# Optimization experiments

Measured on AMD Instinct MI355X. Metric: run time of the kernel, lower is better.

Reference implementation:

```python
import jax, jax.numpy as jnp
import numpy as np

BETA = 1.0  # inverse temperature (default of retrieve())
EPS = 1e-12  # matches torch F.normalize eps


def _l2_normalize(x):
    # torch.nn.functional.normalize(p=2, dim=-1): x / max(||x||, eps)
    n = jnp.sqrt(jnp.sum(x * x, axis=-1, keepdims=True))
    return x / jnp.maximum(n, EPS)


def setup_inputs() -> dict:
    key = jax.random.key(0)
    kq, kk = jax.random.split(key)
    N, K, D = 65536, 4096, 128
    queries = jax.random.normal(kq, (N, D), dtype=jnp.float32)
    # learnable memory keys, init_std = 0.02
    keys = jax.random.normal(kk, (K, D), dtype=jnp.float32) * 0.02
    return {"queries": queries, "keys": keys}


def reference(queries, keys):
    # normalize_keys=True, normalize_queries=True
    k_n = _l2_normalize(keys)
    q_n = _l2_normalize(queries)
    # values are TIED to the raw keys parameter (get_values returns self.keys,
    # un-normalized) — only the score-side keys are normalized.
    values = keys
    scores = BETA * jnp.einsum('nd,kd->nk', q_n, k_n)  # [N, K]
    attention = jax.nn.softmax(scores, axis=-1)
    retrieved = jnp.einsum('nk,kd->nd', attention, values)  # [N, D]
    return retrieved
```

## Files before the change

kernel.cpp:

```cpp
#include <hip/hip_runtime.h>
#include <hip/hip_bf16.h>
#include <stdint.h>


typedef __attribute__((ext_vector_type(8))) short bf16x8;
typedef __attribute__((ext_vector_type(16))) float f32x16;

#define MFMA32(a, b, c) __builtin_amdgcn_mfma_f32_32x32x16_bf16(a, b, c, 0, 0, 0)
#define ASYNC_CP16(gsrc, ldst)                                                  \
  __builtin_amdgcn_global_load_lds(                                             \
      (const __attribute__((address_space(1))) void*)(gsrc),                    \
      (__attribute__((address_space(3))) void*)(ldst), 16, 0, 0)

__device__ __forceinline__ unsigned pkbf(float lo, float hi) {
  union { __hip_bfloat162 h2; unsigned u; } v;
  v.h2 = __float22bfloat162_rn(float2{lo, hi});
  return v.u;
}

__global__ __launch_bounds__(256) void prep_k(const float* __restrict__ k,
                                              char* __restrict__ knf,
                                              char* __restrict__ vtf, int K) {
  __shared__ float sRaw[64 * 132];
  __shared__ float sScale[64];
  const int tid = threadIdx.x;
  const int kbase = blockIdx.x * 64;
  {
    const int key_loc = tid >> 2, dq = tid & 3;
    const float4* src = (const float4*)(k + (size_t)(kbase + key_loc) * 128 + dq * 32);
    float4 f[8];
    float ss = 0.f;
#pragma unroll
    for (int i = 0; i < 8; ++i) {
      f[i] = src[i];
      ss += f[i].x * f[i].x + f[i].y * f[i].y + f[i].z * f[i].z + f[i].w * f[i].w;
    }
    ss += __shfl_xor(ss, 1);
    ss += __shfl_xor(ss, 2);
    float4* dst = (float4*)(sRaw + key_loc * 132 + dq * 32);
#pragma unroll
    for (int i = 0; i < 8; ++i) dst[i] = f[i];
    if (dq == 0) sScale[key_loc] = ss > 0.f ? rsqrtf(ss) : 0.f;
  }
  __syncthreads();

#pragma unroll
  for (int r = 0; r < 4; ++r) {
    const int c = r * 256 + tid;
    const int t_loc = c >> 9, ds = (c >> 6) & 7, l = c & 63;
    const int h5 = l >> 5, c32 = l & 31;
    const int key_loc = t_loc * 32 + c32;
    const float sc = sScale[key_loc];
    const float* p = sRaw + key_loc * 132 + ds * 16 + h5 * 8;
    uint4 w;
    w.x = pkbf(p[0] * sc, p[1] * sc);
    w.y = pkbf(p[2] * sc, p[3] * sc);
    w.z = pkbf(p[4] * sc, p[5] * sc);
    w.w = pkbf(p[6] * sc, p[7] * sc);
    *(uint4*)(knf + ((size_t)blockIdx.x * 1024 + c) * 16) = w;
  }
#pragma unroll
  for (int r = 0; r < 4; ++r) {
    const int c = r * 256 + tid;
    const int s = c >> 8, db2 = (c >> 6) & 3, l = c & 63;
    const int h5 = l >> 5, c32 = l & 31;
    const int d = db2 * 32 + c32;
    const int kb = (s >> 1) * 32 + (s & 1) * 8 + h5 * 4;
    float f[8];
#pragma unroll
    for (int j = 0; j < 8; ++j)
      f[j] = sRaw[(kb + (j & 3) + (j >> 2) * 16) * 132 + d];
    uint4 w;
    w.x = pkbf(f[0], f[1]);
    w.y = pkbf(f[2], f[3]);
    w.z = pkbf(f[4], f[5]);
    w.w = pkbf(f[6], f[7]);
    *(uint4*)(vtf + ((size_t)blockIdx.x * 1024 + c) * 16) = w;
  }
}

__global__ __launch_bounds__(256, 2) void attn_main(
    const float* __restrict__ q, const char* __restrict__ knf,
    const char* __restrict__ vtf, float* __restrict__ out, int K) {
  __shared__ __align__(16) char sK[2][16384];
  const int tid = threadIdx.x;
  const int wave = tid >> 6, lane = tid & 63;
  const int h5 = lane >> 5, c32 = lane & 31;
  const int qrow0 = blockIdx.x * 128 + wave * 32;

  bf16x8 qf[8];
  {
    const float* qr = q + (size_t)(qrow0 + c32) * 128;
    float f[64];
    float ss = 0.f;
#pragma unroll
    for (int ds = 0; ds < 8; ++ds) {
      const float4 a = *(const float4*)(qr + ds * 16 + h5 * 8);
      const float4 b = *(const float4*)(qr + ds * 16 + h5 * 8 + 4);
      f[ds * 8 + 0] = a.x; f[ds * 8 + 1] = a.y; f[ds * 8 + 2] = a.z; f[ds * 8 + 3] = a.w;
      f[ds * 8 + 4] = b.x; f[ds * 8 + 5] = b.y; f[ds * 8 + 6] = b.z; f[ds * 8 + 7] = b.w;
    }
#pragma unroll
    for (int i = 0; i < 64; ++i) ss += f[i] * f[i];
    ss += __shfl_xor(ss, 32);
    const float sc = (ss > 0.f ? rsqrtf(ss) : 0.f) * 1.44269504f;
#pragma unroll
    for (int ds = 0; ds < 8; ++ds) {
      union { unsigned u[4]; bf16x8 v; } t;
#pragma unroll
      for (int p = 0; p < 4; ++p)
        t.u[p] = pkbf(f[ds * 8 + 2 * p] * sc, f[ds * 8 + 2 * p + 1] * sc);
      qf[ds] = t.v;
    }
  }

  f32x16 acc[4];
#pragma unroll
  for (int db2 = 0; db2 < 4; ++db2)
#pragma unroll
    for (int r = 0; r < 16; ++r) acc[db2][r] = 0.f;
  float den = 0.f;

  const int nIter = K >> 6;
  auto stage = [&](int it, int buf) {
#pragma unroll
    for (int i = 0; i < 4; ++i)
      ASYNC_CP16(knf + (size_t)it * 16384 + (wave * 4 + i) * 1024 + lane * 16,
                 sK[buf] + (wave * 4 + i) * 1024);
  };

  stage(0, 0);
  for (int it = 0; it < nIter; ++it) {
    const int buf = it & 1;
    __syncthreads();
    if (it + 1 < nIter) stage(it + 1, buf ^ 1);

    f32x16 S[2];
#pragma unroll
    for (int t = 0; t < 2; ++t) {
      f32x16 s;
#pragma unroll
      for (int r = 0; r < 16; ++r) s[r] = 0.f;
#pragma unroll
      for (int ds = 0; ds < 8; ++ds) {
        const bf16x8 kf = *(const bf16x8*)(sK[buf] + (t * 8 + ds) * 1024 + lane * 16);
        s = MFMA32(kf, qf[ds], s);
      }
      S[t] = s;
    }

    const char* vbase = vtf + (size_t)it * 16384;
    bf16x8 vcur[4], vnxt[4];
#pragma unroll
    for (int db2 = 0; db2 < 4; ++db2)
      vcur[db2] = *(const bf16x8*)(vbase + db2 * 1024 + lane * 16);
#pragma unroll
    for (int s = 0; s < 4; ++s) {
      if (s < 3)
#pragma unroll
        for (int db2 = 0; db2 < 4; ++db2)
          vnxt[db2] = *(const bf16x8*)(vbase + ((s + 1) * 4 + db2) * 1024 + lane * 16);
      const int t = s >> 1, w = s & 1;
      float e[8];
#pragma unroll
      for (int j = 0; j < 8; ++j) {
        const int rr = w * 4 + (j & 3) + (j >> 2) * 8;
        e[j] = __builtin_amdgcn_exp2f(S[t][rr]);
      }
      den += ((e[0] + e[1]) + (e[2] + e[3])) + ((e[4] + e[5]) + (e[6] + e[7]));
      union { unsigned u[4]; bf16x8 v; } pf;
#pragma unroll
      for (int j2 = 0; j2 < 4; ++j2) pf.u[j2] = pkbf(e[2 * j2], e[2 * j2 + 1]);
#pragma unroll
      for (int db2 = 0; db2 < 4; ++db2)
        acc[db2] = MFMA32(vcur[db2], pf.v, acc[db2]);
      if (s < 3)
#pragma unroll
        for (int db2 = 0; db2 < 4; ++db2) vcur[db2] = vnxt[db2];
    }
  }

  den += __shfl_xor(den, 32);
  const float rd = 1.0f / den;

  __syncthreads();
  float* wls = (float*)(&sK[0][0] + wave * 4096);
#pragma unroll
  for (int db2 = 0; db2 < 4; ++db2) {
#pragma unroll
    for (int qd = 0; qd < 4; ++qd) {
      float4 v;
      v.x = acc[db2][qd * 4 + 0] * rd;
      v.y = acc[db2][qd * 4 + 1] * rd;
      v.z = acc[db2][qd * 4 + 2] * rd;
      v.w = acc[db2][qd * 4 + 3] * rd;
      *(float4*)(wls + c32 * 32 + (((h5 + 2 * qd) ^ (c32 & 7)) << 2)) = v;
    }
#pragma unroll
    for (int p = 0; p < 4; ++p) {
      const int ql = p * 8 + (lane >> 3);
      const int x = lane & 7;
      const float4 v = *(const float4*)(wls + ql * 32 + ((x ^ (ql & 7)) << 2));
      *(float4*)(out + (size_t)(qrow0 + ql) * 128 + db2 * 32 + x * 4) = v;
    }
  }
}

extern "C" void kernel_launch(void* const* d_in, const int* in_sizes, int n_in,
                              void* d_out, int out_size, void* d_ws, size_t ws_size,
                              hipStream_t stream) {
  const float* q = (const float*)d_in[0];
  const float* k = (const float*)d_in[1];
  const int N = in_sizes[0] / 128;
  const int K = in_sizes[1] / 128;
  char* ws = (char*)d_ws;
  char* knf = ws;
  char* vtf = ws + (size_t)K * 256;
  float* out = (float*)d_out;

  prep_k<<<dim3(K / 64), dim3(256), 0, stream>>>(k, knf, vtf, K);
  attn_main<<<dim3(N / 128), dim3(256), 0, stream>>>(q, knf, vtf, out, K);
}
```

Baseline: 222.2 us.

## Shrink attention blocks to two waves and process 32 keys per iteration

The main kernel now runs 128-thread blocks covering 64 query rows each, with twice as many blocks, and walks the key dimension 32 keys at a time with 8KB LDS stages instead of 64 keys with 16KB stages. This lowers register and LDS use per block, letting more blocks sit on a CU and shortening each loop body's score live range. The cost is twice as many barriers and iterations, each key tile being reused by only two waves, and more global traffic for the streamed V tiles and K staging.

```diff
diff --git a/kernel.cpp b/kernel.cpp
--- a/kernel.cpp
+++ b/kernel.cpp
@@ -79,14 +79,14 @@
   }
 }
 
-__global__ __launch_bounds__(256, 2) void attn_main(
+__global__ __launch_bounds__(128, 4) void attn_main(
     const float* __restrict__ q, const char* __restrict__ knf,
     const char* __restrict__ vtf, float* __restrict__ out, int K) {
-  __shared__ __align__(16) char sK[2][16384];
+  __shared__ __align__(16) char sK[2][8192];
   const int tid = threadIdx.x;
   const int wave = tid >> 6, lane = tid & 63;
   const int h5 = lane >> 5, c32 = lane & 31;
-  const int qrow0 = blockIdx.x * 128 + wave * 32;
+  const int qrow0 = blockIdx.x * 64 + wave * 32;
 
   bf16x8 qf[8];
   {
@@ -120,13 +120,18 @@
 #pragma unroll
     for (int r = 0; r < 16; ++r) acc[db2][r] = 0.f;
   float den = 0.f;
-
-  const int nIter = K >> 6;
+  f32x16 Zf;
+#pragma unroll
+  for (int r = 0; r < 16; ++r) Zf[r] = 0.f;
+
+  const int nIter = K >> 5;
   auto stage = [&](int it, int buf) {
 #pragma unroll
-    for (int i = 0; i < 4; ++i)
-      ASYNC_CP16(knf + (size_t)it * 16384 + (wave * 4 + i) * 1024 + lane * 16,
-                 sK[buf] + (wave * 4 + i) * 1024);
+    for (int i = 0; i < 4; ++i) {
+      const int ii = wave * 4 + i;
+      ASYNC_CP16(knf + (size_t)it * 8192 + ii * 1024 + lane * 16,
+                 sK[buf] + ii * 1024);
+    }
   };
 
   stage(0, 0);
@@ -135,37 +140,30 @@
     __syncthreads();
     if (it + 1 < nIter) stage(it + 1, buf ^ 1);
 
-    f32x16 S[2];
-#pragma unroll
-    for (int t = 0; t < 2; ++t) {
-      f32x16 s;
-#pragma unroll
-      for (int r = 0; r < 16; ++r) s[r] = 0.f;
-#pragma unroll
-      for (int ds = 0; ds < 8; ++ds) {
-        const bf16x8 kf = *(const bf16x8*)(sK[buf] + (t * 8 + ds) * 1024 + lane * 16);
-        s = MFMA32(kf, qf[ds], s);
-      }
-      S[t] = s;
-    }
-
-    const char* vbase = vtf + (size_t)it * 16384;
+    const char* vbase = vtf + (size_t)it * 8192;
     bf16x8 vcur[4], vnxt[4];
 #pragma unroll
     for (int db2 = 0; db2 < 4; ++db2)
       vcur[db2] = *(const bf16x8*)(vbase + db2 * 1024 + lane * 16);
-#pragma unroll
-    for (int s = 0; s < 4; ++s) {
-      if (s < 3)
+
+    f32x16 S;
+#pragma unroll
+    for (int ds = 0; ds < 8; ++ds) {
+      const bf16x8 kf = *(const bf16x8*)(sK[buf] + ds * 1024 + lane * 16);
+      S = MFMA32(kf, qf[ds], (ds == 0) ? Zf : S);
+    }
+
+#pragma unroll
+    for (int s = 0; s < 2; ++s) {
+      if (s == 0)
 #pragma unroll
         for (int db2 = 0; db2 < 4; ++db2)
-          vnxt[db2] = *(const bf16x8*)(vbase + ((s + 1) * 4 + db2) * 1024 + lane * 16);
-      const int t = s >> 1, w = s & 1;
+          vnxt[db2] = *(const bf16x8*)(vbase + (4 + db2) * 1024 + lane * 16);
       float e[8];
 #pragma unroll
       for (int j = 0; j < 8; ++j) {
-        const int rr = w * 4 + (j & 3) + (j >> 2) * 8;
-        e[j] = __builtin_amdgcn_exp2f(S[t][rr]);
+        const int rr = s * 4 + (j & 3) + (j >> 2) * 8;
+        e[j] = __builtin_amdgcn_exp2f(S[rr]);
       }
       den += ((e[0] + e[1]) + (e[2] + e[3])) + ((e[4] + e[5]) + (e[6] + e[7]));
       union { unsigned u[4]; bf16x8 v; } pf;
@@ -174,7 +172,7 @@
 #pragma unroll
       for (int db2 = 0; db2 < 4; ++db2)
         acc[db2] = MFMA32(vcur[db2], pf.v, acc[db2]);
-      if (s < 3)
+      if (s == 0)
 #pragma unroll
         for (int db2 = 0; db2 < 4; ++db2) vcur[db2] = vnxt[db2];
     }
@@ -219,5 +217,5 @@
   float* out = (float*)d_out;
 
   prep_k<<<dim3(K / 64), dim3(256), 0, stream>>>(k, knf, vtf, K);
-  attn_main<<<dim3(N / 128), dim3(256), 0, stream>>>(q, knf, vtf, out, K);
-}
+  attn_main<<<dim3(N / 64), dim3(128), 0, stream>>>(q, knf, vtf, out, K);
+}
```

Measured after the change: 399.8 us. 1.8x slower.

## Software-pipeline QK scores, exp and PV across key-block iterations

Applied to the files above, without the earlier changes.

Splits the loop body into score computation, exponentiation and PV accumulation. It then skews them so the PV MFMAs of the previous key block are issued between the current block's QK MFMAs and its exp work. The goal is to overlap transcendental and packing ALU work with matrix-core work instead of running them serially inside one iteration. It also seeds the first QK MFMA from a zero constant instead of re-zeroing the accumulator. In exchange it keeps four packed probability fragments live across iterations, which raises register pressure, and it adds a peeled prologue and epilogue.

```diff
diff --git a/kernel.cpp b/kernel.cpp
--- a/kernel.cpp
+++ b/kernel.cpp
@@ -120,6 +120,12 @@
 #pragma unroll
     for (int r = 0; r < 16; ++r) acc[db2][r] = 0.f;
   float den = 0.f;
+  f32x16 Zf;
+#pragma unroll
+  for (int r = 0; r < 16; ++r) Zf[r] = 0.f;
+
+  union pfu { unsigned u[4]; bf16x8 v; };
+  pfu pf[4];
 
   const int nIter = K >> 6;
   auto stage = [&](int it, int buf) {
@@ -129,27 +135,21 @@
                  sK[buf] + (wave * 4 + i) * 1024);
   };
 
-  stage(0, 0);
-  for (int it = 0; it < nIter; ++it) {
-    const int buf = it & 1;
-    __syncthreads();
-    if (it + 1 < nIter) stage(it + 1, buf ^ 1);
-
-    f32x16 S[2];
+  auto computeS = [&](int buf, f32x16* S) {
 #pragma unroll
     for (int t = 0; t < 2; ++t) {
       f32x16 s;
 #pragma unroll
-      for (int r = 0; r < 16; ++r) s[r] = 0.f;
-#pragma unroll
       for (int ds = 0; ds < 8; ++ds) {
         const bf16x8 kf = *(const bf16x8*)(sK[buf] + (t * 8 + ds) * 1024 + lane * 16);
-        s = MFMA32(kf, qf[ds], s);
+        s = MFMA32(kf, qf[ds], (ds == 0) ? Zf : s);
       }
       S[t] = s;
     }
-
-    const char* vbase = vtf + (size_t)it * 16384;
+  };
+
+  auto doPV = [&](int m) {
+    const char* vbase = vtf + (size_t)m * 16384;
     bf16x8 vcur[4], vnxt[4];
 #pragma unroll
     for (int db2 = 0; db2 < 4; ++db2)
@@ -160,6 +160,18 @@
 #pragma unroll
         for (int db2 = 0; db2 < 4; ++db2)
           vnxt[db2] = *(const bf16x8*)(vbase + ((s + 1) * 4 + db2) * 1024 + lane * 16);
+#pragma unroll
+      for (int db2 = 0; db2 < 4; ++db2)
+        acc[db2] = MFMA32(vcur[db2], pf[s].v, acc[db2]);
+      if (s < 3)
+#pragma unroll
+        for (int db2 = 0; db2 < 4; ++db2) vcur[db2] = vnxt[db2];
+    }
+  };
+
+  auto doExp = [&](const f32x16* S) {
+#pragma unroll
+    for (int s = 0; s < 4; ++s) {
       const int t = s >> 1, w = s & 1;
       float e[8];
 #pragma unroll
@@ -168,17 +180,29 @@
         e[j] = __builtin_amdgcn_exp2f(S[t][rr]);
       }
       den += ((e[0] + e[1]) + (e[2] + e[3])) + ((e[4] + e[5]) + (e[6] + e[7]));
-      union { unsigned u[4]; bf16x8 v; } pf;
-#pragma unroll
-      for (int j2 = 0; j2 < 4; ++j2) pf.u[j2] = pkbf(e[2 * j2], e[2 * j2 + 1]);
-#pragma unroll
-      for (int db2 = 0; db2 < 4; ++db2)
-        acc[db2] = MFMA32(vcur[db2], pf.v, acc[db2]);
-      if (s < 3)
-#pragma unroll
-        for (int db2 = 0; db2 < 4; ++db2) vcur[db2] = vnxt[db2];
-    }
-  }
+#pragma unroll
+      for (int j2 = 0; j2 < 4; ++j2) pf[s].u[j2] = pkbf(e[2 * j2], e[2 * j2 + 1]);
+    }
+  };
+
+  stage(0, 0);
+  __syncthreads();
+  stage(1, 1);
+  {
+    f32x16 S[2];
+    computeS(0, S);
+    doExp(S);
+  }
+  for (int it = 1; it < nIter; ++it) {
+    const int buf = it & 1;
+    __syncthreads();
+    if (it + 1 < nIter) stage(it + 1, buf ^ 1);
+    f32x16 S[2];
+    computeS(buf, S);
+    doPV(it - 1);
+    doExp(S);
+  }
+  doPV(nIter - 1);
 
   den += __shfl_xor(den, 32);
   const float rd = 1.0f / den;
```

Measured after the change: 221.5 us. No clear change (-0.3%).

## Split key dimension across two blocks with separate reduction kernel

Applied to the files above, without the earlier changes.

Splits the K loop into two halves handled by separate blocks (gridDim.y=2). Each half writes unnormalized numerators and denominators, and a new reduce kernel sums and normalizes them. Occupancy is raised to 3 blocks per SU, and the V register double-buffering is removed to free registers. The cost is extra global traffic for a second N×128 numerator, the denominators, and one more launch.

```diff
diff --git a/kernel.cpp b/kernel.cpp
--- a/kernel.cpp
+++ b/kernel.cpp
@@ -79,13 +79,15 @@
   }
 }
 
-__global__ __launch_bounds__(256, 2) void attn_main(
+__global__ __launch_bounds__(256, 3) void attn_main(
     const float* __restrict__ q, const char* __restrict__ knf,
-    const char* __restrict__ vtf, float* __restrict__ out, int K) {
+    const char* __restrict__ vtf, float* __restrict__ num0,
+    float* __restrict__ num1, float* __restrict__ den, int N, int K) {
   __shared__ __align__(16) char sK[2][16384];
   const int tid = threadIdx.x;
   const int wave = tid >> 6, lane = tid & 63;
   const int h5 = lane >> 5, c32 = lane & 31;
+  const int split = blockIdx.y;
   const int qrow0 = blockIdx.x * 128 + wave * 32;
 
   bf16x8 qf[8];
@@ -119,47 +121,41 @@
   for (int db2 = 0; db2 < 4; ++db2)
 #pragma unroll
     for (int r = 0; r < 16; ++r) acc[db2][r] = 0.f;
-  float den = 0.f;
-
-  const int nIter = K >> 6;
-  auto stage = [&](int it, int buf) {
+  float denv = 0.f;
+  f32x16 Zf;
+#pragma unroll
+  for (int r = 0; r < 16; ++r) Zf[r] = 0.f;
+
+  const int iBeg = split * (K >> 7);
+  const int nIter = K >> 7;
+  auto stage = [&](int m, int buf) {
 #pragma unroll
     for (int i = 0; i < 4; ++i)
-      ASYNC_CP16(knf + (size_t)it * 16384 + (wave * 4 + i) * 1024 + lane * 16,
+      ASYNC_CP16(knf + (size_t)m * 16384 + (wave * 4 + i) * 1024 + lane * 16,
                  sK[buf] + (wave * 4 + i) * 1024);
   };
 
-  stage(0, 0);
+  stage(iBeg, 0);
   for (int it = 0; it < nIter; ++it) {
     const int buf = it & 1;
     __syncthreads();
-    if (it + 1 < nIter) stage(it + 1, buf ^ 1);
+    if (it + 1 < nIter) stage(iBeg + it + 1, buf ^ 1);
 
     f32x16 S[2];
 #pragma unroll
     for (int t = 0; t < 2; ++t) {
       f32x16 s;
 #pragma unroll
-      for (int r = 0; r < 16; ++r) s[r] = 0.f;
-#pragma unroll
       for (int ds = 0; ds < 8; ++ds) {
         const bf16x8 kf = *(const bf16x8*)(sK[buf] + (t * 8 + ds) * 1024 + lane * 16);
-        s = MFMA32(kf, qf[ds], s);
+        s = MFMA32(kf, qf[ds], (ds == 0) ? Zf : s);
       }
       S[t] = s;
     }
 
-    const char* vbase = vtf + (size_t)it * 16384;
-    bf16x8 vcur[4], vnxt[4];
-#pragma unroll
-    for (int db2 = 0; db2 < 4; ++db2)
-      vcur[db2] = *(const bf16x8*)(vbase + db2 * 1024 + lane * 16);
+    const char* vbase = vtf + (size_t)(iBeg + it) * 16384;
 #pragma unroll
     for (int s = 0; s < 4; ++s) {
-      if (s < 3)
-#pragma unroll
-        for (int db2 = 0; db2 < 4; ++db2)
-          vnxt[db2] = *(const bf16x8*)(vbase + ((s + 1) * 4 + db2) * 1024 + lane * 16);
       const int t = s >> 1, w = s & 1;
       float e[8];
 #pragma unroll
@@ -167,21 +163,21 @@
         const int rr = w * 4 + (j & 3) + (j >> 2) * 8;
         e[j] = __builtin_amdgcn_exp2f(S[t][rr]);
       }
-      den += ((e[0] + e[1]) + (e[2] + e[3])) + ((e[4] + e[5]) + (e[6] + e[7]));
+      denv += ((e[0] + e[1]) + (e[2] + e[3])) + ((e[4] + e[5]) + (e[6] + e[7]));
       union { unsigned u[4]; bf16x8 v; } pf;
 #pragma unroll
       for (int j2 = 0; j2 < 4; ++j2) pf.u[j2] = pkbf(e[2 * j2], e[2 * j2 + 1]);
 #pragma unroll
-      for (int db2 = 0; db2 < 4; ++db2)
-        acc[db2] = MFMA32(vcur[db2], pf.v, acc[db2]);
-      if (s < 3)
-#pragma unroll
-        for (int db2 = 0; db2 < 4; ++db2) vcur[db2] = vnxt[db2];
-    }
-  }
-
-  den += __shfl_xor(den, 32);
-  const float rd = 1.0f / den;
+      for (int db2 = 0; db2 < 4; ++db2) {
+        const bf16x8 vf = *(const bf16x8*)(vbase + (s * 4 + db2) * 1024 + lane * 16);
+        acc[db2] = MFMA32(vf, pf.v, acc[db2]);
+      }
+    }
+  }
+
+  denv += __shfl_xor(denv, 32);
+  float* numout = split ? num1 : num0;
+  if (h5 == 0) den[(size_t)split * N + qrow0 + c32] = denv;
 
   __syncthreads();
   float* wls = (float*)(&sK[0][0] + wave * 4096);
@@ -190,10 +186,10 @@
 #pragma unroll
     for (int qd = 0; qd < 4; ++qd) {
       float4 v;
-      v.x = acc[db2][qd * 4 + 0] * rd;
-      v.y = acc[db2][qd * 4 + 1] * rd;
-      v.z = acc[db2][qd * 4 + 2] * rd;
-      v.w = acc[db2][qd * 4 + 3] * rd;
+      v.x = acc[db2][qd * 4 + 0];
+      v.y = acc[db2][qd * 4 + 1];
+      v.z = acc[db2][qd * 4 + 2];
+      v.w = acc[db2][qd * 4 + 3];
       *(float4*)(wls + c32 * 32 + (((h5 + 2 * qd) ^ (c32 & 7)) << 2)) = v;
     }
 #pragma unroll
@@ -201,9 +197,25 @@
       const int ql = p * 8 + (lane >> 3);
       const int x = lane & 7;
       const float4 v = *(const float4*)(wls + ql * 32 + ((x ^ (ql & 7)) << 2));
-      *(float4*)(out + (size_t)(qrow0 + ql) * 128 + db2 * 32 + x * 4) = v;
-    }
-  }
+      *(float4*)(numout + (size_t)(qrow0 + ql) * 128 + db2 * 32 + x * 4) = v;
+    }
+  }
+}
+
+__global__ __launch_bounds__(256) void reduce_k(const float4* __restrict__ num1,
+                                                const float* __restrict__ den,
+                                                float4* __restrict__ out, int N) {
+  const size_t f = (size_t)blockIdx.x * 256 + threadIdx.x;
+  const size_t row = f >> 5;
+  const float rd = 1.0f / (den[row] + den[(size_t)N + row]);
+  const float4 a = out[f];
+  const float4 b = num1[f];
+  float4 o;
+  o.x = (a.x + b.x) * rd;
+  o.y = (a.y + b.y) * rd;
+  o.z = (a.z + b.z) * rd;
+  o.w = (a.w + b.w) * rd;
+  out[f] = o;
 }
 
 extern "C" void kernel_launch(void* const* d_in, const int* in_sizes, int n_in,
@@ -216,8 +228,13 @@
   char* ws = (char*)d_ws;
   char* knf = ws;
   char* vtf = ws + (size_t)K * 256;
+  float* den = (float*)(ws + 2 * 1024 * 1024);
+  float* num1 = (float*)(ws + 4 * 1024 * 1024);
   float* out = (float*)d_out;
 
   prep_k<<<dim3(K / 64), dim3(256), 0, stream>>>(k, knf, vtf, K);
-  attn_main<<<dim3(N / 128), dim3(256), 0, stream>>>(q, knf, vtf, out, K);
-}
+  attn_main<<<dim3(N / 128, 2), dim3(256), 0, stream>>>(q, knf, vtf, out, num1,
+                                                        den, N, K);
+  reduce_k<<<dim3(N * 32 / 256), dim3(256), 0, stream>>>((const float4*)num1,
+                                                         den, (float4*)out, N);
+}
```

Measured after the change: 250.1 us. 12.5% more time.
